# Performance work log

Hardware: AMD Instinct MI355X
Metric: run time of the kernel (lower is better)

Reference implementation:

```python
import math
import jax, jax.numpy as jnp
import numpy as np

N_HEADS = 12
D_EMBED = 768
BATCH = 2
SEQ = 2048


def setup_inputs() -> dict:
    key = jax.random.key(0)
    ks = jax.random.split(key, 5)
    scale = 0.02
    return {
        "x": jax.random.normal(ks[0], (BATCH, SEQ, D_EMBED), dtype=jnp.float32),
        "w_in": jax.random.normal(ks[1], (D_EMBED, 3 * D_EMBED), dtype=jnp.float32) * scale,
        "b_in": jax.random.normal(ks[2], (3 * D_EMBED,), dtype=jnp.float32) * scale,
        "w_out": jax.random.normal(ks[3], (D_EMBED, D_EMBED), dtype=jnp.float32) * scale,
        "b_out": jax.random.normal(ks[4], (D_EMBED,), dtype=jnp.float32) * scale,
    }


def reference(x, w_in, b_in, w_out, b_out):
    # x: [B, S, D]
    B, S, D = x.shape
    H = N_HEADS
    dh = D // H
    # Fused QKV projection: [B, S, 3D]
    qkv = x @ w_in + b_in
    q, k, v = jnp.split(qkv, 3, axis=-1)
    # [B, S, D] -> [B, H, S, dh]
    def to_heads(t):
        return t.reshape(B, S, H, dh).transpose(0, 2, 1, 3)
    q, k, v = to_heads(q), to_heads(k), to_heads(v)
    # Scaled dot-product attention (non-causal, masked=False default)
    scale = 1.0 / math.sqrt(dh)
    scores = jnp.einsum("bhqd,bhkd->bhqk", q, k) * scale  # [B, H, S, S]
    probs = jax.nn.softmax(scores, axis=-1)
    out = jnp.einsum("bhqk,bhkd->bhqd", probs, v)  # [B, H, S, dh]
    # Merge heads: [B, S, D]
    out = out.transpose(0, 2, 1, 3).reshape(B, S, D)
    return out @ w_out + b_out
```

## Files before the change

kernel.cpp:

```cpp
#include <hip/hip_runtime.h>
#include <stdint.h>

#define B_   2
#define S_   2048
#define D_   768
#define H_   12
#define DH_  64
#define N3_  2304
#define M_   4096

typedef __attribute__((ext_vector_type(8))) short    bf16x8;
typedef __attribute__((ext_vector_type(4))) float    f32x4;
typedef __attribute__((ext_vector_type(4))) int      i32x4;
typedef __attribute__((ext_vector_type(4))) unsigned short u16x4;
typedef _Float16 f16x4 __attribute__((ext_vector_type(4)));
typedef __fp16   h16x2 __attribute__((ext_vector_type(2)));

#define KSCALE 0.18033688011112042f

__device__ inline unsigned short f2bf(float f) {
    union { float f; unsigned u; } v; v.f = f;
    unsigned r = v.u + 0x7FFFu + ((v.u >> 16) & 1u);
    return (unsigned short)(r >> 16);
}

__device__ inline void async_copy16(const void* g, void* l) {
    __builtin_amdgcn_global_load_lds((const __attribute__((address_space(1))) void*)g,
                                     (__attribute__((address_space(3))) void*)l, 16, 0, 0);
}

__global__ void cvt_bf16(const float* __restrict__ in, unsigned short* __restrict__ out, int n4) {
    int i = blockIdx.x * blockDim.x + threadIdx.x;
    if (i >= n4) return;
    f32x4 v = *(const f32x4*)(in + (size_t)i * 4);
    u16x4 o;
    o.x = f2bf(v.x); o.y = f2bf(v.y); o.z = f2bf(v.z); o.w = f2bf(v.w);
    *(u16x4*)(out + (size_t)i * 4) = o;
}

__global__ void transpose_bf16(const float* __restrict__ in, unsigned short* __restrict__ out,
                               int R, int C) {
    __shared__ unsigned short t[32][33];
    int c0 = blockIdx.x * 32, r0 = blockIdx.y * 32;
    int tx = threadIdx.x, ty = threadIdx.y;
#pragma unroll
    for (int j = 0; j < 4; j++)
        t[ty + j * 8][tx] = f2bf(in[(size_t)(r0 + ty + j * 8) * C + c0 + tx]);
    __syncthreads();
#pragma unroll
    for (int j = 0; j < 4; j++)
        out[(size_t)(c0 + ty + j * 8) * R + r0 + tx] = t[tx][ty + j * 8];
}

__global__ void vtrans(const unsigned short* __restrict__ V, unsigned short* __restrict__ Vt) {
    __shared__ unsigned short t[64 * 65];
    const int bid = blockIdx.x;
    const int bh  = bid >> 5;
    const int s0  = (bid & 31) * 64;
    const int tid = threadIdx.x;
    const unsigned short* src = V  + (size_t)bh * S_ * DH_ + (size_t)s0 * DH_;
    unsigned short*       dst = Vt + (size_t)bh * DH_ * S_ + s0;
#pragma unroll
    for (int p = 0; p < 2; p++) {
        int c = p * 256 + tid;
        int s = c >> 3, dc = c & 7;
        i32x4 v = *(const i32x4*)&src[s * 64 + dc * 8];
        const unsigned short* e = (const unsigned short*)&v;
#pragma unroll
        for (int j = 0; j < 8; j++) t[(dc * 8 + j) * 65 + s] = e[j];
    }
    __syncthreads();
#pragma unroll
    for (int p = 0; p < 2; p++) {
        int c = p * 256 + tid;
        int d = c >> 3, sc = c & 7;
        unsigned short tmp[8];
#pragma unroll
        for (int j = 0; j < 8; j++) tmp[j] = t[d * 65 + sc * 8 + j];
        *(i32x4*)&dst[(size_t)d * S_ + sc * 8] = *(const i32x4*)tmp;
    }
}

__global__ __launch_bounds__(256) void gemm_qkv(
    const unsigned short* __restrict__ A,
    const unsigned short* __restrict__ Bt,
    const float* __restrict__ bias,
    unsigned short* __restrict__ QK,
    unsigned short* __restrict__ Vnat)
{
    __shared__ __align__(16) short Al[128 * 32];
    __shared__ __align__(16) short Bl[96 * 32];

    const int tid  = threadIdx.x;
    const int w    = tid >> 6;
    const int lane = tid & 63;
    const int r    = lane & 15;
    const int quad = lane >> 4;
    const int m0   = blockIdx.y * 128;
    const int n0   = blockIdx.x * 96;
    const int wm   = (w & 1) * 64;
    const int wn   = (w >> 1) * 48;
    const int K    = D_;

    f32x4 acc[4][3];
#pragma unroll
    for (int i = 0; i < 4; i++)
#pragma unroll
        for (int j = 0; j < 3; j++) acc[i][j] = f32x4{0.f, 0.f, 0.f, 0.f};

    const int c0 = tid, c1 = tid + 256, cb1 = tid + 256;
    const size_t ga0 = (size_t)(m0 + (c0 >> 2)) * K + (c0 & 3) * 8;
    const size_t ga1 = (size_t)(m0 + (c1 >> 2)) * K + (c1 & 3) * 8;
    const size_t gb0 = (size_t)(n0 + (c0 >> 2)) * K + (c0 & 3) * 8;
    const size_t gb1 = (size_t)(n0 + (cb1 >> 2)) * K + (cb1 & 3) * 8;
    short* lA0 = &Al[(0 * 256 + w * 64) * 8];
    short* lA1 = &Al[(1 * 256 + w * 64) * 8];
    short* lB0 = &Bl[(0 * 256 + w * 64) * 8];
    short* lB1 = &Bl[(1 * 256 + w * 64) * 8];

    for (int k0 = 0; k0 < K; k0 += 32) {
        __syncthreads();
        async_copy16(A  + ga0 + k0, lA0);
        async_copy16(A  + ga1 + k0, lA1);
        async_copy16(Bt + gb0 + k0, lB0);
        if (w < 2) async_copy16(Bt + gb1 + k0, lB1);
        __syncthreads();

        bf16x8 af[4], bf[3];
#pragma unroll
        for (int mi = 0; mi < 4; mi++)
            af[mi] = *(const bf16x8*)&Al[(wm + mi * 16 + r) * 32 + quad * 8];
#pragma unroll
        for (int ni = 0; ni < 3; ni++)
            bf[ni] = *(const bf16x8*)&Bl[(wn + ni * 16 + r) * 32 + quad * 8];
#pragma unroll
        for (int mi = 0; mi < 4; mi++)
#pragma unroll
            for (int ni = 0; ni < 3; ni++)
                acc[mi][ni] = __builtin_amdgcn_mfma_f32_16x16x32_bf16(
                    af[mi], bf[ni], acc[mi][ni], 0, 0, 0);
    }

    const size_t one = (size_t)B_ * H_ * S_ * DH_;
#pragma unroll
    for (int ni = 0; ni < 3; ni++) {
        int col  = n0 + wn + ni * 16 + r;
        float bv = bias[col];
        int part = col / 768;
        int cc   = col - part * 768;
        int h    = cc >> 6;
        int d    = cc & 63;
        float scl = (part == 1) ? KSCALE : 1.0f;
        unsigned short* dst = (part == 2) ? Vnat : (QK + (size_t)part * one);
#pragma unroll
        for (int mi = 0; mi < 4; mi++) {
#pragma unroll
            for (int i = 0; i < 4; i++) {
                int row = m0 + wm + mi * 16 + quad * 4 + i;
                int b   = row >> 11;
                int s   = row & 2047;
                float v = (acc[mi][ni][i] + bv) * scl;
                unsigned short bits;
                if (part == 2) {
                    union { _Float16 h; unsigned short s; } cv;
                    cv.h = (_Float16)v;
                    bits = cv.s;
                } else {
                    bits = f2bf(v);
                }
                dst[(((size_t)(b * H_ + h)) * S_ + s) * DH_ + d] = bits;
            }
        }
    }
}

__global__ __launch_bounds__(256) void gemm_out(
    const unsigned short* __restrict__ A,
    const unsigned short* __restrict__ Bt,
    const float* __restrict__ bias,
    float* __restrict__ Cf)
{
    __shared__ __align__(16) short Al[64 * 32];
    __shared__ __align__(16) short Bl[64 * 32];

    const int tid  = threadIdx.x;
    const int w    = tid >> 6;
    const int lane = tid & 63;
    const int r    = lane & 15;
    const int quad = lane >> 4;
    const int m0   = blockIdx.y * 64;
    const int n0   = blockIdx.x * 64;
    const int wm   = (w & 1) * 32;
    const int wn   = (w >> 1) * 32;
    const int K    = D_;
    const int N    = D_;

    f32x4 acc[2][2];
#pragma unroll
    for (int i = 0; i < 2; i++)
#pragma unroll
        for (int j = 0; j < 2; j++) acc[i][j] = f32x4{0.f, 0.f, 0.f, 0.f};

    const size_t ga = (size_t)(m0 + (tid >> 2)) * K + (tid & 3) * 8;
    const size_t gb = (size_t)(n0 + (tid >> 2)) * K + (tid & 3) * 8;
    short* lA = &Al[(w * 64) * 8];
    short* lB = &Bl[(w * 64) * 8];

    for (int k0 = 0; k0 < K; k0 += 32) {
        __syncthreads();
        async_copy16(A  + ga + k0, lA);
        async_copy16(Bt + gb + k0, lB);
        __syncthreads();

        bf16x8 af[2], bf[2];
#pragma unroll
        for (int mi = 0; mi < 2; mi++)
            af[mi] = *(const bf16x8*)&Al[(wm + mi * 16 + r) * 32 + quad * 8];
#pragma unroll
        for (int ni = 0; ni < 2; ni++)
            bf[ni] = *(const bf16x8*)&Bl[(wn + ni * 16 + r) * 32 + quad * 8];
#pragma unroll
        for (int mi = 0; mi < 2; mi++)
#pragma unroll
            for (int ni = 0; ni < 2; ni++)
                acc[mi][ni] = __builtin_amdgcn_mfma_f32_16x16x32_bf16(
                    af[mi], bf[ni], acc[mi][ni], 0, 0, 0);
    }

#pragma unroll
    for (int ni = 0; ni < 2; ni++) {
        int col  = n0 + wn + ni * 16 + r;
        float bv = bias[col];
#pragma unroll
        for (int mi = 0; mi < 2; mi++) {
#pragma unroll
            for (int i = 0; i < 4; i++) {
                int row = m0 + wm + mi * 16 + quad * 4 + i;
                Cf[(size_t)row * N + col] = acc[mi][ni][i] + bv;
            }
        }
    }
}

__global__ __launch_bounds__(256) void attn_kernel(
    const unsigned short* __restrict__ Q,
    const unsigned short* __restrict__ K,
    const unsigned short* __restrict__ Vt,
    unsigned short* __restrict__ On0,
    unsigned short* __restrict__ On1,
    float* __restrict__ lbuf)
{
    __shared__ __align__(16) short Kl[64 * 64];
    __shared__ __align__(16) short Vl[64 * 64];

    const int tid  = threadIdx.x;
    const int w    = tid >> 6;
    const int lane = tid & 63;
    const int r    = lane & 15;
    const int quad = lane >> 4;
    const int xk   = r & 7;
    const int bid  = blockIdx.x;
    const int bh   = bid % 24;
    const int t2   = bid / 24;
    const int qb   = t2 & 15;
    const int half = t2 >> 4;
    const size_t baseQK = (size_t)bh * S_ * DH_;
    const size_t baseV  = (size_t)bh * DH_ * S_;
    const int q0   = qb * 128;
    const int kt0  = half * 16;

    bf16x8 qf[2][2];
#pragma unroll
    for (int qt = 0; qt < 2; qt++) {
        const unsigned short* qp =
            Q + baseQK + (size_t)(q0 + w * 32 + qt * 16 + r) * DH_ + quad * 8;
        qf[qt][0] = *(const bf16x8*)(qp);
        qf[qt][1] = *(const bf16x8*)(qp + 32);
    }

    f32x4 o[2][4];
    f32x4 lacc[2];
#pragma unroll
    for (int qt = 0; qt < 2; qt++) {
        lacc[qt] = f32x4{0.f, 0.f, 0.f, 0.f};
#pragma unroll
        for (int nb = 0; nb < 4; nb++) o[qt][nb] = f32x4{0.f, 0.f, 0.f, 0.f};
    }

    const f16x4 ONES = {(_Float16)1.f, (_Float16)1.f, (_Float16)1.f, (_Float16)1.f};

    const int srw = tid >> 3, schk = tid & 7;
    const unsigned short* kg = K  + baseQK + (size_t)kt0 * 4096 + tid * 8;
    const unsigned short* vg = Vt + baseV + (size_t)kt0 * 64 + (size_t)srw * S_ + schk * 8;
    const int lb = srw * 64 + (schk ^ (srw & 7)) * 8;

    i32x4 kreg[2], vreg[2];
    kreg[0] = *(const i32x4*)(kg);
    kreg[1] = *(const i32x4*)(kg + 2048);
    vreg[0] = *(const i32x4*)(vg);
    vreg[1] = *(const i32x4*)(vg + 32 * S_);

    for (int it = 0; it < 16; it++) {
        __syncthreads();
        *(i32x4*)&Kl[lb]        = kreg[0];
        *(i32x4*)&Kl[lb + 2048] = kreg[1];
        *(i32x4*)&Vl[lb]        = vreg[0];
        *(i32x4*)&Vl[lb + 2048] = vreg[1];
        __syncthreads();

        if (it != 15) {
            const unsigned short* kn = kg + (it + 1) * 4096;
            const unsigned short* vn = vg + (it + 1) * 64;
            kreg[0] = *(const i32x4*)(kn);
            kreg[1] = *(const i32x4*)(kn + 2048);
            vreg[0] = *(const i32x4*)(vn);
            vreg[1] = *(const i32x4*)(vn + 32 * S_);
        }

        f32x4 sa[2][4];
#pragma unroll
        for (int qt = 0; qt < 2; qt++)
#pragma unroll
            for (int kb = 0; kb < 4; kb++) sa[qt][kb] = f32x4{0.f, 0.f, 0.f, 0.f};
#pragma unroll
        for (int t = 0; t < 2; t++)
#pragma unroll
            for (int kb = 0; kb < 4; kb++) {
                bf16x8 kf = *(const bf16x8*)&Kl[(kb * 16 + r) * 64 + ((t * 4 + quad) ^ xk) * 8];
#pragma unroll
                for (int qt = 0; qt < 2; qt++)
                    sa[qt][kb] = __builtin_amdgcn_mfma_f32_16x16x32_bf16(
                        kf, qf[qt][t], sa[qt][kb], 0, 0, 0);
            }

        f16x4 pf[2][4];
#pragma unroll
        for (int qt = 0; qt < 2; qt++)
#pragma unroll
            for (int kb = 0; kb < 4; kb++) {
                float p0 = __builtin_amdgcn_exp2f(sa[qt][kb][0]);
                float p1 = __builtin_amdgcn_exp2f(sa[qt][kb][1]);
                float p2 = __builtin_amdgcn_exp2f(sa[qt][kb][2]);
                float p3 = __builtin_amdgcn_exp2f(sa[qt][kb][3]);
                union { f16x4 v; h16x2 h[2]; } u;
                u.h[0] = __builtin_amdgcn_cvt_pkrtz(p0, p1);
                u.h[1] = __builtin_amdgcn_cvt_pkrtz(p2, p3);
                pf[qt][kb] = u.v;
            }

#pragma unroll
        for (int kb = 0; kb < 4; kb++) {
#pragma unroll
            for (int nb = 0; nb < 4; nb++) {
                f16x4 vf = *(const f16x4*)&Vl[(nb * 16 + r) * 64 +
                                              ((kb * 2 + (quad >> 1)) ^ xk) * 8 + (quad & 1) * 4];
#pragma unroll
                for (int qt = 0; qt < 2; qt++)
                    o[qt][nb] = __builtin_amdgcn_mfma_f32_16x16x16f16(
                        pf[qt][kb], vf, o[qt][nb], 0, 0, 0);
            }
#pragma unroll
            for (int qt = 0; qt < 2; qt++)
                lacc[qt] = __builtin_amdgcn_mfma_f32_16x16x16f16(
                    pf[qt][kb], ONES, lacc[qt], 0, 0, 0);
        }
    }

    unsigned short* Ob = half ? On1 : On0;
#pragma unroll
    for (int qt = 0; qt < 2; qt++)
#pragma unroll
        for (int i = 0; i < 4; i++) {
            int s = q0 + w * 32 + qt * 16 + quad * 4 + i;
            size_t row = (size_t)bh * S_ + s;
            if (r == 0) lbuf[half * (24 * S_) + row] = lacc[qt][i];
#pragma unroll
            for (int nb = 0; nb < 4; nb++) {
                union { _Float16 h; unsigned short u; } cv;
                cv.h = (_Float16)o[qt][nb][i];
                Ob[row * 64 + nb * 16 + r] = cv.u;
            }
        }
}

__global__ void combine_attn(const unsigned short* __restrict__ On0,
                             const unsigned short* __restrict__ On1,
                             const float* __restrict__ lbuf,
                             unsigned short* __restrict__ Out)
{
    int g   = blockIdx.x * 256 + threadIdx.x;
    int hd8 = g % 96;
    int bs  = g / 96;
    int h   = hd8 >> 3;
    int d8  = (hd8 & 7) * 8;
    size_t row = ((size_t)((bs >> 11) * H_ + h)) * S_ + (bs & 2047);
    float inv = 1.0f / (lbuf[row] + lbuf[24 * S_ + row]);
    i32x4 a = *(const i32x4*)&On0[row * 64 + d8];
    i32x4 c = *(const i32x4*)&On1[row * 64 + d8];
    const _Float16* fa = (const _Float16*)&a;
    const _Float16* fc = (const _Float16*)&c;
    unsigned short tmp[8];
#pragma unroll
    for (int j = 0; j < 8; j++)
        tmp[j] = f2bf(((float)fa[j] + (float)fc[j]) * inv);
    *(i32x4*)&Out[(size_t)bs * D_ + h * 64 + d8] = *(const i32x4*)tmp;
}

extern "C" void kernel_launch(void* const* d_in, const int* in_sizes, int n_in,
                              void* d_out, int out_size, void* d_ws, size_t ws_size,
                              hipStream_t stream) {
    const float* x     = (const float*)d_in[0];
    const float* w_in  = (const float*)d_in[1];
    const float* b_in  = (const float*)d_in[2];
    const float* w_out = (const float*)d_in[3];
    const float* b_out = (const float*)d_in[4];
    float* out = (float*)d_out;
    char* ws = (char*)d_ws;

    unsigned short* xb    = (unsigned short*)(ws);
    unsigned short* winT  = (unsigned short*)(ws + 6291456);
    unsigned short* woutT = (unsigned short*)(ws + 9830400);
    unsigned short* QKV   = (unsigned short*)(ws + 11010048);
    unsigned short* tmpV  = (unsigned short*)(ws + 29884416);

    const size_t one = (size_t)B_ * H_ * S_ * DH_;
    unsigned short* Vtbuf = QKV + 2 * one;
    unsigned short* On0   = xb;
    unsigned short* On1   = tmpV;
    float*          lbuf  = (float*)winT;
    unsigned short* attnO = QKV;

    cvt_bf16<<<3072, 256, 0, stream>>>(x, xb, (M_ * D_) / 4);
    transpose_bf16<<<dim3(N3_ / 32, D_ / 32), dim3(32, 8), 0, stream>>>(w_in, winT, D_, N3_);
    transpose_bf16<<<dim3(D_ / 32, D_ / 32), dim3(32, 8), 0, stream>>>(w_out, woutT, D_, D_);

    gemm_qkv<<<dim3(N3_ / 96, M_ / 128), 256, 0, stream>>>(
        xb, winT, b_in, QKV, tmpV);

    vtrans<<<24 * 32, 256, 0, stream>>>(tmpV, Vtbuf);

    attn_kernel<<<24 * 16 * 2, 256, 0, stream>>>(
        QKV, QKV + one, Vtbuf, On0, On1, lbuf);

    combine_attn<<<1536, 256, 0, stream>>>(On0, On1, lbuf, attnO);

    gemm_out<<<dim3(D_ / 64, M_ / 64), 256, 0, stream>>>(
        attnO, woutT, b_out, out);
}
```

Before: 167.1 us.

## Merge prep kernels into one launch and write V transposed from QKV GEMM

Three preprocessing launches (x conversion and two weight transposes) are merged into a single kernel that selects its job by block index. The separate V transpose kernel is removed: the QKV GEMM epilogue now writes V directly in [b,h,d,s] layout, packing four consecutive sequence positions into one 8-byte store. This removes two kernel launches and one extra read/write pass over V, at the cost of more scattered stores in the GEMM epilogue.

```diff
diff --git a/kernel.cpp b/kernel.cpp
--- a/kernel.cpp
+++ b/kernel.cpp
@@ -29,56 +29,33 @@
                                      (__attribute__((address_space(3))) void*)l, 16, 0, 0);
 }
 
-__global__ void cvt_bf16(const float* __restrict__ in, unsigned short* __restrict__ out, int n4) {
-    int i = blockIdx.x * blockDim.x + threadIdx.x;
-    if (i >= n4) return;
-    f32x4 v = *(const f32x4*)(in + (size_t)i * 4);
-    u16x4 o;
-    o.x = f2bf(v.x); o.y = f2bf(v.y); o.z = f2bf(v.z); o.w = f2bf(v.w);
-    *(u16x4*)(out + (size_t)i * 4) = o;
-}
-
-__global__ void transpose_bf16(const float* __restrict__ in, unsigned short* __restrict__ out,
-                               int R, int C) {
+__global__ __launch_bounds__(256) void prep_all(
+    const float* __restrict__ x, const float* __restrict__ w_in,
+    const float* __restrict__ w_out,
+    unsigned short* __restrict__ xb, unsigned short* __restrict__ winT,
+    unsigned short* __restrict__ woutT)
+{
     __shared__ unsigned short t[32][33];
-    int c0 = blockIdx.x * 32, r0 = blockIdx.y * 32;
-    int tx = threadIdx.x, ty = threadIdx.y;
+    const int gid = blockIdx.x, tid = threadIdx.x;
+    if (gid < 3072) {
+        int i = gid * 256 + tid;
+        f32x4 v = *(const f32x4*)(x + (size_t)i * 4);
+        u16x4 o;
+        o.x = f2bf(v.x); o.y = f2bf(v.y); o.z = f2bf(v.z); o.w = f2bf(v.w);
+        *(u16x4*)(xb + (size_t)i * 4) = o;
+        return;
+    }
+    const float* src; unsigned short* dst; int R, C, bx, by;
+    if (gid < 4800) { int b = gid - 3072; src = w_in;  dst = winT;  R = D_; C = N3_; bx = b % 72; by = b / 72; }
+    else            { int b = gid - 4800; src = w_out; dst = woutT; R = D_; C = D_;  bx = b % 24; by = b / 24; }
+    int c0 = bx * 32, r0 = by * 32, tx = tid & 31, ty = tid >> 5;
 #pragma unroll
     for (int j = 0; j < 4; j++)
-        t[ty + j * 8][tx] = f2bf(in[(size_t)(r0 + ty + j * 8) * C + c0 + tx]);
+        t[ty + j * 8][tx] = f2bf(src[(size_t)(r0 + ty + j * 8) * C + c0 + tx]);
     __syncthreads();
 #pragma unroll
     for (int j = 0; j < 4; j++)
-        out[(size_t)(c0 + ty + j * 8) * R + r0 + tx] = t[tx][ty + j * 8];
-}
-
-__global__ void vtrans(const unsigned short* __restrict__ V, unsigned short* __restrict__ Vt) {
-    __shared__ unsigned short t[64 * 65];
-    const int bid = blockIdx.x;
-    const int bh  = bid >> 5;
-    const int s0  = (bid & 31) * 64;
-    const int tid = threadIdx.x;
-    const unsigned short* src = V  + (size_t)bh * S_ * DH_ + (size_t)s0 * DH_;
-    unsigned short*       dst = Vt + (size_t)bh * DH_ * S_ + s0;
-#pragma unroll
-    for (int p = 0; p < 2; p++) {
-        int c = p * 256 + tid;
-        int s = c >> 3, dc = c & 7;
-        i32x4 v = *(const i32x4*)&src[s * 64 + dc * 8];
-        const unsigned short* e = (const unsigned short*)&v;
-#pragma unroll
-        for (int j = 0; j < 8; j++) t[(dc * 8 + j) * 65 + s] = e[j];
-    }
-    __syncthreads();
-#pragma unroll
-    for (int p = 0; p < 2; p++) {
-        int c = p * 256 + tid;
-        int d = c >> 3, sc = c & 7;
-        unsigned short tmp[8];
-#pragma unroll
-        for (int j = 0; j < 8; j++) tmp[j] = t[d * 65 + sc * 8 + j];
-        *(i32x4*)&dst[(size_t)d * S_ + sc * 8] = *(const i32x4*)tmp;
-    }
+        dst[(size_t)(c0 + ty + j * 8) * R + r0 + tx] = t[tx][ty + j * 8];
 }
 
 __global__ __launch_bounds__(256) void gemm_qkv(
@@ -86,7 +63,7 @@
     const unsigned short* __restrict__ Bt,
     const float* __restrict__ bias,
     unsigned short* __restrict__ QK,
-    unsigned short* __restrict__ Vnat)
+    unsigned short* __restrict__ Vt)
 {
     __shared__ __align__(16) short Al[128 * 32];
     __shared__ __align__(16) short Bl[96 * 32];
@@ -108,11 +85,11 @@
 #pragma unroll
         for (int j = 0; j < 3; j++) acc[i][j] = f32x4{0.f, 0.f, 0.f, 0.f};
 
-    const int c0 = tid, c1 = tid + 256, cb1 = tid + 256;
+    const int c0 = tid, c1 = tid + 256;
     const size_t ga0 = (size_t)(m0 + (c0 >> 2)) * K + (c0 & 3) * 8;
     const size_t ga1 = (size_t)(m0 + (c1 >> 2)) * K + (c1 & 3) * 8;
     const size_t gb0 = (size_t)(n0 + (c0 >> 2)) * K + (c0 & 3) * 8;
-    const size_t gb1 = (size_t)(n0 + (cb1 >> 2)) * K + (cb1 & 3) * 8;
+    const size_t gb1 = (size_t)(n0 + (c1 >> 2)) * K + (c1 & 3) * 8;
     short* lA0 = &Al[(0 * 256 + w * 64) * 8];
     short* lA1 = &Al[(1 * 256 + w * 64) * 8];
     short* lB0 = &Bl[(0 * 256 + w * 64) * 8];
@@ -150,25 +127,34 @@
         int cc   = col - part * 768;
         int h    = cc >> 6;
         int d    = cc & 63;
-        float scl = (part == 1) ? KSCALE : 1.0f;
-        unsigned short* dst = (part == 2) ? Vnat : (QK + (size_t)part * one);
-#pragma unroll
-        for (int mi = 0; mi < 4; mi++) {
-#pragma unroll
-            for (int i = 0; i < 4; i++) {
-                int row = m0 + wm + mi * 16 + quad * 4 + i;
-                int b   = row >> 11;
-                int s   = row & 2047;
-                float v = (acc[mi][ni][i] + bv) * scl;
-                unsigned short bits;
-                if (part == 2) {
+        if (part == 2) {
+#pragma unroll
+            for (int mi = 0; mi < 4; mi++) {
+                int row0 = m0 + wm + mi * 16 + quad * 4;
+                int b    = row0 >> 11;
+                int s0   = row0 & 2047;
+                u16x4 pk;
+#pragma unroll
+                for (int i = 0; i < 4; i++) {
                     union { _Float16 h; unsigned short s; } cv;
-                    cv.h = (_Float16)v;
-                    bits = cv.s;
-                } else {
-                    bits = f2bf(v);
+                    cv.h = (_Float16)(acc[mi][ni][i] + bv);
+                    pk[i] = cv.s;
                 }
-                dst[(((size_t)(b * H_ + h)) * S_ + s) * DH_ + d] = bits;
+                *(u16x4*)&Vt[(((size_t)(b * H_ + h)) * DH_ + d) * S_ + s0] = pk;
+            }
+        } else {
+            float scl = (part == 1) ? KSCALE : 1.0f;
+            unsigned short* dst = QK + (size_t)part * one;
+#pragma unroll
+            for (int mi = 0; mi < 4; mi++) {
+#pragma unroll
+                for (int i = 0; i < 4; i++) {
+                    int row = m0 + wm + mi * 16 + quad * 4 + i;
+                    int b   = row >> 11;
+                    int s   = row & 2047;
+                    dst[(((size_t)(b * H_ + h)) * S_ + s) * DH_ + d] =
+                        f2bf((acc[mi][ni][i] + bv) * scl);
+                }
             }
         }
     }
@@ -421,23 +407,18 @@
     unsigned short* winT  = (unsigned short*)(ws + 6291456);
     unsigned short* woutT = (unsigned short*)(ws + 9830400);
     unsigned short* QKV   = (unsigned short*)(ws + 11010048);
-    unsigned short* tmpV  = (unsigned short*)(ws + 29884416);
+    unsigned short* On1   = (unsigned short*)(ws + 29884416);
 
     const size_t one = (size_t)B_ * H_ * S_ * DH_;
     unsigned short* Vtbuf = QKV + 2 * one;
     unsigned short* On0   = xb;
-    unsigned short* On1   = tmpV;
     float*          lbuf  = (float*)winT;
     unsigned short* attnO = QKV;
 
-    cvt_bf16<<<3072, 256, 0, stream>>>(x, xb, (M_ * D_) / 4);
-    transpose_bf16<<<dim3(N3_ / 32, D_ / 32), dim3(32, 8), 0, stream>>>(w_in, winT, D_, N3_);
-    transpose_bf16<<<dim3(D_ / 32, D_ / 32), dim3(32, 8), 0, stream>>>(w_out, woutT, D_, D_);
+    prep_all<<<5376, 256, 0, stream>>>(x, w_in, w_out, xb, winT, woutT);
 
     gemm_qkv<<<dim3(N3_ / 96, M_ / 128), 256, 0, stream>>>(
-        xb, winT, b_in, QKV, tmpV);
-
-    vtrans<<<24 * 32, 256, 0, stream>>>(tmpV, Vtbuf);
+        xb, winT, b_in, QKV, Vtbuf);
 
     attn_kernel<<<24 * 16 * 2, 256, 0, stream>>>(
         QKV, QKV + one, Vtbuf, On0, On1, lbuf);
```

After: 158.9 us. -4.9%, faster.
